# Performance work log

Measured on AMD Instinct MI355X. Metric: run time of the kernel, lower is better.

## Reference

```python
import jax, jax.numpy as jnp
import numpy as np

TOP_K_PERCENT = 0.7


def setup_inputs() -> dict:
    key = jax.random.key(0)
    k1, k2, k3, k4 = jax.random.split(key, 4)
    B, C, H, W = 4, 19, 512, 1024
    logits = jax.random.normal(k1, (B, C, H, W), dtype=jnp.float32)
    labels = jax.random.randint(k2, (B, H, W), 0, C, dtype=jnp.int64)
    smooth_labels = jax.random.uniform(k3, (B, C, H, W), dtype=jnp.float32)
    weight2 = jax.random.uniform(k4, (C,), dtype=jnp.float32)
    return {"logits": logits, "labels": labels, "smooth_labels": smooth_labels, "weight2": weight2}


def reference(logits, labels, smooth_labels, weight2):
    # Fused equivalent of the per-class loop:
    #   cum[b,h,w] = sum_c smooth[b,c,h,w] * weight2[c] * (-log_softmax(logits)[b,c,h,w])
    # (ignore_label=-1 never matches any class index, so no masking occurs.)
    logp = jax.nn.log_softmax(logits, axis=1)  # [B,C,H,W]
    w = weight2[None, :, None, None]
    pixel_losses_2 = -(smooth_labels * w * logp).sum(axis=1)  # [B,H,W]
    flat = pixel_losses_2.reshape(-1)
    k = int(TOP_K_PERCENT * flat.shape[0])  # static shape -> python int
    top_vals, _ = jax.lax.top_k(flat, k)
    return top_vals.mean()
```

## Files before the change

kernel.cpp:

```cpp
#include <hip/hip_runtime.h>

#define NPIX     2097152
#define NT4      524288
#define NCH      19
#define KSEL     1468006u
#define NBLK     2048
#define H1B      4096
#define H23B     1024
#define NHB      128

#define OFF_ROWS  (NPIX*4)
#define OFF_COMB1 (OFF_ROWS + NHB*H1B*4)
#define OFF_COMB2 (OFF_COMB1 + H1B*4)
#define OFF_PART  (OFF_COMB2 + H23B*4)
#define OFF_CTRL  (OFF_PART + NBLK*8)

struct Ctrl { unsigned p1, n1, p2, n2, T, r2; };

__global__ __launch_bounds__(256) void k_loss(
    const float* __restrict__ logits, const float* __restrict__ smooth,
    const float* __restrict__ wgt, float* __restrict__ loss)
{
    int tid = blockIdx.x * 256 + threadIdx.x;
    int img = tid >> 17;
    int rem = tid & 131071;
    const float4* L = (const float4*)logits + (size_t)img * (NCH * 131072) + rem;
    const float4* S = (const float4*)smooth + (size_t)img * (NCH * 131072) + rem;

    float4 xb[4], sb[4];
    #pragma unroll
    for (int i = 0; i < 4; ++i) {
        xb[i] = L[(size_t)i * 131072];
        sb[i] = S[(size_t)i * 131072];
    }

    float m0 = -3.4e38f, m1 = -3.4e38f, m2 = -3.4e38f, m3 = -3.4e38f;
    float s0 = 0.f, s1 = 0.f, s2 = 0.f, s3 = 0.f;
    float sw0 = 0.f, sw1 = 0.f, sw2 = 0.f, sw3 = 0.f;
    float swl0 = 0.f, swl1 = 0.f, swl2 = 0.f, swl3 = 0.f;

    #pragma unroll
    for (int c = 0; c < NCH; ++c) {
        float4 xv = xb[c & 3];
        float4 sv = sb[c & 3];
        if (c + 4 < NCH) {
            xb[c & 3] = L[(size_t)(c + 4) * 131072];
            sb[c & 3] = S[(size_t)(c + 4) * 131072];
        }
        float wc = wgt[c];

        float n0 = fmaxf(m0, xv.x), n1 = fmaxf(m1, xv.y);
        float n2 = fmaxf(m2, xv.z), n3 = fmaxf(m3, xv.w);
        s0 = s0 * __expf(m0 - n0) + __expf(xv.x - n0);
        s1 = s1 * __expf(m1 - n1) + __expf(xv.y - n1);
        s2 = s2 * __expf(m2 - n2) + __expf(xv.z - n2);
        s3 = s3 * __expf(m3 - n3) + __expf(xv.w - n3);
        m0 = n0; m1 = n1; m2 = n2; m3 = n3;

        float t0 = sv.x * wc, t1 = sv.y * wc, t2 = sv.z * wc, t3 = sv.w * wc;
        sw0 += t0; sw1 += t1; sw2 += t2; sw3 += t3;
        swl0 += t0 * xv.x; swl1 += t1 * xv.y;
        swl2 += t2 * xv.z; swl3 += t3 * xv.w;
    }

    float l0 = fmaxf((m0 + __logf(s0)) * sw0 - swl0, 0.f);
    float l1 = fmaxf((m1 + __logf(s1)) * sw1 - swl1, 0.f);
    float l2 = fmaxf((m2 + __logf(s2)) * sw2 - swl2, 0.f);
    float l3 = fmaxf((m3 + __logf(s3)) * sw3 - swl3, 0.f);

    ((float4*)loss)[tid] = make_float4(l0, l1, l2, l3);
}

__global__ __launch_bounds__(256) void k_hist1(
    const uint4* __restrict__ lossbits, unsigned* __restrict__ rows)
{
    __shared__ unsigned h[H1B];
    int t = threadIdx.x;
    #pragma unroll
    for (int j = t; j < H1B; j += 256) h[j] = 0;
    __syncthreads();
    int base = blockIdx.x * (NT4 / NHB);
    for (int i = t; i < NT4 / NHB; i += 256) {
        uint4 v = lossbits[base + i];
        atomicAdd(&h[v.x >> 20], 1u);
        atomicAdd(&h[v.y >> 20], 1u);
        atomicAdd(&h[v.z >> 20], 1u);
        atomicAdd(&h[v.w >> 20], 1u);
    }
    __syncthreads();
    for (int j = t; j < H1B; j += 256)
        rows[blockIdx.x * H1B + j] = h[j];
}

__global__ __launch_bounds__(256) void k_histr(
    const uint4* __restrict__ lossbits, const Ctrl* __restrict__ ctrl,
    unsigned* __restrict__ rows, int lvl)
{
    __shared__ unsigned h[H23B];
    unsigned pref = (lvl == 0) ? ctrl->p1 : ctrl->p2;
    int ms = (lvl == 0) ? 20 : 10;
    int bs = (lvl == 0) ? 10 : 0;
    int t = threadIdx.x;
    #pragma unroll
    for (int j = t; j < H23B; j += 256) h[j] = 0;
    __syncthreads();
    int base = blockIdx.x * (NT4 / NHB);
    for (int i = t; i < NT4 / NHB; i += 256) {
        uint4 v = lossbits[base + i];
        if ((v.x >> ms) == pref) atomicAdd(&h[(v.x >> bs) & 1023u], 1u);
        if ((v.y >> ms) == pref) atomicAdd(&h[(v.y >> bs) & 1023u], 1u);
        if ((v.z >> ms) == pref) atomicAdd(&h[(v.z >> bs) & 1023u], 1u);
        if ((v.w >> ms) == pref) atomicAdd(&h[(v.w >> bs) & 1023u], 1u);
    }
    __syncthreads();
    for (int j = t; j < H23B; j += 256)
        rows[blockIdx.x * H23B + j] = h[j];
}

__global__ __launch_bounds__(256) void k_reduce(
    const unsigned* __restrict__ rows, unsigned* __restrict__ comb, int nbins)
{
    int i = blockIdx.x * 256 + threadIdx.x;
    unsigned s = 0;
    for (int b = 0; b < NHB; ++b) s += rows[b * nbins + i];
    comb[i] = s;
}

__global__ __launch_bounds__(256) void k_sel1(
    const unsigned* __restrict__ comb, Ctrl* __restrict__ ctrl)
{
    __shared__ unsigned bins[H1B];
    __shared__ unsigned cs[256];
    __shared__ unsigned sh_t0, sh_base;
    int t = threadIdx.x;
    for (int j = t; j < H1B; j += 256) bins[j] = comb[j];
    __syncthreads();
    unsigned sum = 0;
    #pragma unroll
    for (int j = 0; j < 16; ++j) sum += bins[t * 16 + j];
    cs[t] = sum; __syncthreads();
    for (int off = 1; off < 256; off <<= 1) {
        unsigned v = (t + off < 256) ? cs[t + off] : 0u;
        __syncthreads();
        cs[t] += v;
        __syncthreads();
    }
    unsigned St = cs[t], Sn = (t < 255) ? cs[t + 1] : 0u;
    if (St >= KSEL && Sn < KSEL) { sh_t0 = (unsigned)t; sh_base = Sn; }
    __syncthreads();
    if (t == 0) {
        unsigned cum = sh_base;
        for (int b = (int)sh_t0 * 16 + 15;; --b) {
            unsigned c = bins[b];
            if (cum + c >= KSEL) { ctrl->p1 = (unsigned)b; ctrl->n1 = KSEL - cum; break; }
            cum += c;
        }
    }
}

__global__ __launch_bounds__(256) void k_selr(
    const unsigned* __restrict__ comb, Ctrl* __restrict__ ctrl, int lvl)
{
    __shared__ unsigned bins[H23B];
    __shared__ unsigned cs[256];
    __shared__ unsigned sh_t0, sh_base;
    int t = threadIdx.x;
    unsigned need = (lvl == 0) ? ctrl->n1 : ctrl->n2;
    unsigned pref = (lvl == 0) ? ctrl->p1 : ctrl->p2;
    for (int j = t; j < H23B; j += 256) bins[j] = comb[j];
    __syncthreads();
    unsigned sum = bins[t*4] + bins[t*4+1] + bins[t*4+2] + bins[t*4+3];
    cs[t] = sum; __syncthreads();
    for (int off = 1; off < 256; off <<= 1) {
        unsigned v = (t + off < 256) ? cs[t + off] : 0u;
        __syncthreads();
        cs[t] += v;
        __syncthreads();
    }
    unsigned St = cs[t], Sn = (t < 255) ? cs[t + 1] : 0u;
    if (St >= need && Sn < need) { sh_t0 = (unsigned)t; sh_base = Sn; }
    __syncthreads();
    if (t == 0) {
        unsigned cum = sh_base;
        for (int b = (int)sh_t0 * 4 + 3;; --b) {
            unsigned c = bins[b];
            if (cum + c >= need) {
                if (lvl == 0) { ctrl->p2 = (pref << 10) | (unsigned)b; ctrl->n2 = need - cum; }
                else          { ctrl->T  = (pref << 10) | (unsigned)b; ctrl->r2 = need - cum; }
                break;
            }
            cum += c;
        }
    }
}

__global__ __launch_bounds__(256) void k_sum(
    const uint4* __restrict__ lossbits, const Ctrl* __restrict__ ctrl,
    double* __restrict__ partials)
{
    unsigned T = ctrl->T;
    int tid = blockIdx.x * 256 + threadIdx.x;
    uint4 v = lossbits[tid];
    double acc = 0.0;
    if (v.x > T) acc += (double)__uint_as_float(v.x);
    if (v.y > T) acc += (double)__uint_as_float(v.y);
    if (v.z > T) acc += (double)__uint_as_float(v.z);
    if (v.w > T) acc += (double)__uint_as_float(v.w);
    #pragma unroll
    for (int off = 32; off > 0; off >>= 1) acc += __shfl_down(acc, off, 64);
    __shared__ double wsum[4];
    int lane = threadIdx.x & 63, wid = threadIdx.x >> 6;
    if (lane == 0) wsum[wid] = acc;
    __syncthreads();
    if (threadIdx.x == 0)
        partials[blockIdx.x] = wsum[0] + wsum[1] + wsum[2] + wsum[3];
}

__global__ __launch_bounds__(256) void k_final(
    const double* __restrict__ partials, const Ctrl* __restrict__ ctrl,
    float* __restrict__ out)
{
    double acc = 0.0;
    for (int i = threadIdx.x; i < NBLK; i += 256) acc += partials[i];
    #pragma unroll
    for (int off = 32; off > 0; off >>= 1) acc += __shfl_down(acc, off, 64);
    __shared__ double wsum[4];
    int lane = threadIdx.x & 63, wid = threadIdx.x >> 6;
    if (lane == 0) wsum[wid] = acc;
    __syncthreads();
    if (threadIdx.x == 0) {
        double tot = wsum[0] + wsum[1] + wsum[2] + wsum[3];
        tot += (double)ctrl->r2 * (double)__uint_as_float(ctrl->T);
        out[0] = (float)(tot / (double)KSEL);
    }
}

extern "C" void kernel_launch(void* const* d_in, const int* in_sizes, int n_in,
                              void* d_out, int out_size, void* d_ws, size_t ws_size,
                              hipStream_t stream)
{
    const float* logits = (const float*)d_in[0];
    const float* smooth = (const float*)d_in[2];
    const float* wgt    = (const float*)d_in[3];

    char* ws = (char*)d_ws;
    float*    loss     = (float*)ws;
    unsigned* rows     = (unsigned*)(ws + OFF_ROWS);
    unsigned* comb1    = (unsigned*)(ws + OFF_COMB1);
    unsigned* comb2    = (unsigned*)(ws + OFF_COMB2);
    double*   partials = (double*)(ws + OFF_PART);
    Ctrl*     ctrl     = (Ctrl*)(ws + OFF_CTRL);
    const uint4* lb    = (const uint4*)loss;

    k_loss  <<<NBLK, 256, 0, stream>>>(logits, smooth, wgt, loss);
    k_hist1 <<<NHB, 256, 0, stream>>>(lb, rows);
    k_reduce<<<H1B / 256, 256, 0, stream>>>(rows, comb1, H1B);
    k_sel1  <<<1, 256, 0, stream>>>(comb1, ctrl);
    k_histr <<<NHB, 256, 0, stream>>>(lb, ctrl, rows, 0);
    k_reduce<<<H23B / 256, 256, 0, stream>>>(rows, comb2, H23B);
    k_selr  <<<1, 256, 0, stream>>>(comb2, ctrl, 0);
    k_histr <<<NHB, 256, 0, stream>>>(lb, ctrl, rows, 1);
    k_reduce<<<H23B / 256, 256, 0, stream>>>(rows, comb2, H23B);
    k_selr  <<<1, 256, 0, stream>>>(comb2, ctrl, 1);
    k_sum   <<<NBLK, 256, 0, stream>>>(lb, ctrl, partials);
    k_final <<<1, 256, 0, stream>>>(partials, ctrl, (float*)d_out);
}
```

Baseline: 377.9 us.

## Fuse radix-select passes, use global atomics for histograms, merge final sum

Restructures the top-k radix select pipeline. Per-block histogram rows and the separate reduce kernels are replaced by global atomic accumulation, with the bins zeroed inside the loss kernel. The third histogram pass is fused with the above-threshold sum, and the final selection is folded into the finish kernel, cutting the launch count from twelve to seven and dropping one full read of the loss array. The loss kernel now handles two pixels per thread (float2) across more blocks, and histogram grids grow to 512 blocks. The tradeoff is contention on the global atomics.

```diff
diff --git a/kernel.cpp b/kernel.cpp
--- a/kernel.cpp
+++ b/kernel.cpp
@@ -1,87 +1,86 @@
 #include <hip/hip_runtime.h>
 
-#define NPIX     2097152
-#define NT4      524288
-#define NCH      19
-#define KSEL     1468006u
-#define NBLK     2048
-#define H1B      4096
-#define H23B     1024
-#define NHB      128
-
-#define OFF_ROWS  (NPIX*4)
-#define OFF_COMB1 (OFF_ROWS + NHB*H1B*4)
+#define NPIX 2097152
+#define NT2  1048576
+#define NT4  524288
+#define NCH  19
+#define CPL2 262144
+#define KSEL 1468006u
+#define LBLK 4096
+#define HB   512
+#define H1B  4096
+#define H2B  1024
+
+#define OFF_COMB1 (NPIX*4)
 #define OFF_COMB2 (OFF_COMB1 + H1B*4)
-#define OFF_PART  (OFF_COMB2 + H23B*4)
-#define OFF_CTRL  (OFF_PART + NBLK*8)
-
-struct Ctrl { unsigned p1, n1, p2, n2, T, r2; };
-
-__global__ __launch_bounds__(256) void k_loss(
+#define OFF_PART  (OFF_COMB2 + H2B*4)
+#define OFF_CTRL  (OFF_PART + HB*8)
+
+struct Ctrl { unsigned p1, n1, p2, n2; };
+
+__global__ __launch_bounds__(256, 8) void k_loss(
     const float* __restrict__ logits, const float* __restrict__ smooth,
-    const float* __restrict__ wgt, float* __restrict__ loss)
-{
+    const float* __restrict__ wgt, float* __restrict__ loss,
+    unsigned* __restrict__ combz)
+{
+    if (blockIdx.x == 0) {
+        for (int j = threadIdx.x; j < H1B + H2B; j += 256) combz[j] = 0u;
+    }
     int tid = blockIdx.x * 256 + threadIdx.x;
-    int img = tid >> 17;
-    int rem = tid & 131071;
-    const float4* L = (const float4*)logits + (size_t)img * (NCH * 131072) + rem;
-    const float4* S = (const float4*)smooth + (size_t)img * (NCH * 131072) + rem;
-
-    float4 xb[4], sb[4];
+    int img = tid >> 18;
+    int rem = tid & (CPL2 - 1);
+    const float2* L = (const float2*)logits + (size_t)img * (NCH * CPL2) + rem;
+    const float2* S = (const float2*)smooth + (size_t)img * (NCH * CPL2) + rem;
+
+    float2 xb[4], sb[4];
     #pragma unroll
     for (int i = 0; i < 4; ++i) {
-        xb[i] = L[(size_t)i * 131072];
-        sb[i] = S[(size_t)i * 131072];
-    }
-
-    float m0 = -3.4e38f, m1 = -3.4e38f, m2 = -3.4e38f, m3 = -3.4e38f;
-    float s0 = 0.f, s1 = 0.f, s2 = 0.f, s3 = 0.f;
-    float sw0 = 0.f, sw1 = 0.f, sw2 = 0.f, sw3 = 0.f;
-    float swl0 = 0.f, swl1 = 0.f, swl2 = 0.f, swl3 = 0.f;
+        xb[i] = L[(size_t)i * CPL2];
+        sb[i] = S[(size_t)i * CPL2];
+    }
+
+    float m0 = -3.4e38f, m1 = -3.4e38f;
+    float s0 = 0.f, s1 = 0.f;
+    float sw0 = 0.f, sw1 = 0.f;
+    float swl0 = 0.f, swl1 = 0.f;
 
     #pragma unroll
     for (int c = 0; c < NCH; ++c) {
-        float4 xv = xb[c & 3];
-        float4 sv = sb[c & 3];
+        float2 xv = xb[c & 3];
+        float2 sv = sb[c & 3];
         if (c + 4 < NCH) {
-            xb[c & 3] = L[(size_t)(c + 4) * 131072];
-            sb[c & 3] = S[(size_t)(c + 4) * 131072];
+            xb[c & 3] = L[(size_t)(c + 4) * CPL2];
+            sb[c & 3] = S[(size_t)(c + 4) * CPL2];
         }
         float wc = wgt[c];
 
         float n0 = fmaxf(m0, xv.x), n1 = fmaxf(m1, xv.y);
-        float n2 = fmaxf(m2, xv.z), n3 = fmaxf(m3, xv.w);
         s0 = s0 * __expf(m0 - n0) + __expf(xv.x - n0);
         s1 = s1 * __expf(m1 - n1) + __expf(xv.y - n1);
-        s2 = s2 * __expf(m2 - n2) + __expf(xv.z - n2);
-        s3 = s3 * __expf(m3 - n3) + __expf(xv.w - n3);
-        m0 = n0; m1 = n1; m2 = n2; m3 = n3;
-
-        float t0 = sv.x * wc, t1 = sv.y * wc, t2 = sv.z * wc, t3 = sv.w * wc;
-        sw0 += t0; sw1 += t1; sw2 += t2; sw3 += t3;
+        m0 = n0; m1 = n1;
+
+        float t0 = sv.x * wc, t1 = sv.y * wc;
+        sw0 += t0; sw1 += t1;
         swl0 += t0 * xv.x; swl1 += t1 * xv.y;
-        swl2 += t2 * xv.z; swl3 += t3 * xv.w;
     }
 
     float l0 = fmaxf((m0 + __logf(s0)) * sw0 - swl0, 0.f);
     float l1 = fmaxf((m1 + __logf(s1)) * sw1 - swl1, 0.f);
-    float l2 = fmaxf((m2 + __logf(s2)) * sw2 - swl2, 0.f);
-    float l3 = fmaxf((m3 + __logf(s3)) * sw3 - swl3, 0.f);
-
-    ((float4*)loss)[tid] = make_float4(l0, l1, l2, l3);
+    ((float2*)loss)[tid] = make_float2(l0, l1);
 }
 
 __global__ __launch_bounds__(256) void k_hist1(
-    const uint4* __restrict__ lossbits, unsigned* __restrict__ rows)
+    const uint4* __restrict__ lb, unsigned* __restrict__ comb1)
 {
     __shared__ unsigned h[H1B];
     int t = threadIdx.x;
     #pragma unroll
     for (int j = t; j < H1B; j += 256) h[j] = 0;
     __syncthreads();
-    int base = blockIdx.x * (NT4 / NHB);
-    for (int i = t; i < NT4 / NHB; i += 256) {
-        uint4 v = lossbits[base + i];
+    int base = blockIdx.x * (NT4 / HB);
+    #pragma unroll
+    for (int i = 0; i < NT4 / HB / 256; ++i) {
+        uint4 v = lb[base + i * 256 + t];
         atomicAdd(&h[v.x >> 20], 1u);
         atomicAdd(&h[v.y >> 20], 1u);
         atomicAdd(&h[v.z >> 20], 1u);
@@ -89,41 +88,7 @@
     }
     __syncthreads();
     for (int j = t; j < H1B; j += 256)
-        rows[blockIdx.x * H1B + j] = h[j];
-}
-
-__global__ __launch_bounds__(256) void k_histr(
-    const uint4* __restrict__ lossbits, const Ctrl* __restrict__ ctrl,
-    unsigned* __restrict__ rows, int lvl)
-{
-    __shared__ unsigned h[H23B];
-    unsigned pref = (lvl == 0) ? ctrl->p1 : ctrl->p2;
-    int ms = (lvl == 0) ? 20 : 10;
-    int bs = (lvl == 0) ? 10 : 0;
-    int t = threadIdx.x;
-    #pragma unroll
-    for (int j = t; j < H23B; j += 256) h[j] = 0;
-    __syncthreads();
-    int base = blockIdx.x * (NT4 / NHB);
-    for (int i = t; i < NT4 / NHB; i += 256) {
-        uint4 v = lossbits[base + i];
-        if ((v.x >> ms) == pref) atomicAdd(&h[(v.x >> bs) & 1023u], 1u);
-        if ((v.y >> ms) == pref) atomicAdd(&h[(v.y >> bs) & 1023u], 1u);
-        if ((v.z >> ms) == pref) atomicAdd(&h[(v.z >> bs) & 1023u], 1u);
-        if ((v.w >> ms) == pref) atomicAdd(&h[(v.w >> bs) & 1023u], 1u);
-    }
-    __syncthreads();
-    for (int j = t; j < H23B; j += 256)
-        rows[blockIdx.x * H23B + j] = h[j];
-}
-
-__global__ __launch_bounds__(256) void k_reduce(
-    const unsigned* __restrict__ rows, unsigned* __restrict__ comb, int nbins)
-{
-    int i = blockIdx.x * 256 + threadIdx.x;
-    unsigned s = 0;
-    for (int b = 0; b < NHB; ++b) s += rows[b * nbins + i];
-    comb[i] = s;
+        if (h[j]) atomicAdd(&comb1[j], h[j]);
 }
 
 __global__ __launch_bounds__(256) void k_sel1(
@@ -158,16 +123,39 @@
     }
 }
 
-__global__ __launch_bounds__(256) void k_selr(
-    const unsigned* __restrict__ comb, Ctrl* __restrict__ ctrl, int lvl)
-{
-    __shared__ unsigned bins[H23B];
+__global__ __launch_bounds__(256) void k_hist2(
+    const uint4* __restrict__ lb, const Ctrl* __restrict__ ctrl,
+    unsigned* __restrict__ comb2)
+{
+    __shared__ unsigned h[H2B];
+    unsigned p1 = ctrl->p1;
+    int t = threadIdx.x;
+    #pragma unroll
+    for (int j = t; j < H2B; j += 256) h[j] = 0;
+    __syncthreads();
+    int base = blockIdx.x * (NT4 / HB);
+    #pragma unroll
+    for (int i = 0; i < NT4 / HB / 256; ++i) {
+        uint4 v = lb[base + i * 256 + t];
+        if ((v.x >> 20) == p1) atomicAdd(&h[(v.x >> 10) & 1023u], 1u);
+        if ((v.y >> 20) == p1) atomicAdd(&h[(v.y >> 10) & 1023u], 1u);
+        if ((v.z >> 20) == p1) atomicAdd(&h[(v.z >> 10) & 1023u], 1u);
+        if ((v.w >> 20) == p1) atomicAdd(&h[(v.w >> 10) & 1023u], 1u);
+    }
+    __syncthreads();
+    for (int j = t; j < H2B; j += 256)
+        if (h[j]) atomicAdd(&comb2[j], h[j]);
+}
+
+__global__ __launch_bounds__(256) void k_sel2(
+    unsigned* __restrict__ comb2, Ctrl* __restrict__ ctrl)
+{
+    __shared__ unsigned bins[H2B];
     __shared__ unsigned cs[256];
     __shared__ unsigned sh_t0, sh_base;
     int t = threadIdx.x;
-    unsigned need = (lvl == 0) ? ctrl->n1 : ctrl->n2;
-    unsigned pref = (lvl == 0) ? ctrl->p1 : ctrl->p2;
-    for (int j = t; j < H23B; j += 256) bins[j] = comb[j];
+    unsigned need = ctrl->n1, pref = ctrl->p1;
+    for (int j = t; j < H2B; j += 256) { bins[j] = comb2[j]; comb2[j] = 0u; }
     __syncthreads();
     unsigned sum = bins[t*4] + bins[t*4+1] + bins[t*4+2] + bins[t*4+3];
     cs[t] = sum; __syncthreads();
@@ -185,8 +173,8 @@
         for (int b = (int)sh_t0 * 4 + 3;; --b) {
             unsigned c = bins[b];
             if (cum + c >= need) {
-                if (lvl == 0) { ctrl->p2 = (pref << 10) | (unsigned)b; ctrl->n2 = need - cum; }
-                else          { ctrl->T  = (pref << 10) | (unsigned)b; ctrl->r2 = need - cum; }
+                ctrl->p2 = (pref << 10) | (unsigned)b;
+                ctrl->n2 = need - cum;
                 break;
             }
             cum += c;
@@ -194,43 +182,92 @@
     }
 }
 
-__global__ __launch_bounds__(256) void k_sum(
-    const uint4* __restrict__ lossbits, const Ctrl* __restrict__ ctrl,
-    double* __restrict__ partials)
-{
-    unsigned T = ctrl->T;
-    int tid = blockIdx.x * 256 + threadIdx.x;
-    uint4 v = lossbits[tid];
+__global__ __launch_bounds__(256) void k_hist3(
+    const uint4* __restrict__ lb, const Ctrl* __restrict__ ctrl,
+    unsigned* __restrict__ comb2, double* __restrict__ partials)
+{
+    __shared__ unsigned h[H2B];
+    __shared__ double wsum[4];
+    unsigned p2 = ctrl->p2;
+    int t = threadIdx.x;
+    #pragma unroll
+    for (int j = t; j < H2B; j += 256) h[j] = 0;
+    __syncthreads();
+    int base = blockIdx.x * (NT4 / HB);
     double acc = 0.0;
-    if (v.x > T) acc += (double)__uint_as_float(v.x);
-    if (v.y > T) acc += (double)__uint_as_float(v.y);
-    if (v.z > T) acc += (double)__uint_as_float(v.z);
-    if (v.w > T) acc += (double)__uint_as_float(v.w);
+    #pragma unroll
+    for (int i = 0; i < NT4 / HB / 256; ++i) {
+        uint4 v = lb[base + i * 256 + t];
+        unsigned px = v.x >> 10, py = v.y >> 10, pz = v.z >> 10, pw = v.w >> 10;
+        if (px == p2) atomicAdd(&h[v.x & 1023u], 1u);
+        else if (px > p2) acc += (double)__uint_as_float(v.x);
+        if (py == p2) atomicAdd(&h[v.y & 1023u], 1u);
+        else if (py > p2) acc += (double)__uint_as_float(v.y);
+        if (pz == p2) atomicAdd(&h[v.z & 1023u], 1u);
+        else if (pz > p2) acc += (double)__uint_as_float(v.z);
+        if (pw == p2) atomicAdd(&h[v.w & 1023u], 1u);
+        else if (pw > p2) acc += (double)__uint_as_float(v.w);
+    }
+    __syncthreads();
+    for (int j = t; j < H2B; j += 256)
+        if (h[j]) atomicAdd(&comb2[j], h[j]);
     #pragma unroll
     for (int off = 32; off > 0; off >>= 1) acc += __shfl_down(acc, off, 64);
+    int lane = t & 63, wid = t >> 6;
+    if (lane == 0) wsum[wid] = acc;
+    __syncthreads();
+    if (t == 0) partials[blockIdx.x] = wsum[0] + wsum[1] + wsum[2] + wsum[3];
+}
+
+__global__ __launch_bounds__(256) void k_fin(
+    const unsigned* __restrict__ comb2, const double* __restrict__ partials,
+    const Ctrl* __restrict__ ctrl, float* __restrict__ out)
+{
+    __shared__ unsigned bins[H2B];
+    __shared__ unsigned cs[256];
+    __shared__ unsigned sh_t0, sh_base, sh_b3, sh_r2;
     __shared__ double wsum[4];
-    int lane = threadIdx.x & 63, wid = threadIdx.x >> 6;
+    int t = threadIdx.x;
+    unsigned need = ctrl->n2, p2 = ctrl->p2;
+    for (int j = t; j < H2B; j += 256) bins[j] = comb2[j];
+    __syncthreads();
+    unsigned sum = bins[t*4] + bins[t*4+1] + bins[t*4+2] + bins[t*4+3];
+    cs[t] = sum; __syncthreads();
+    for (int off = 1; off < 256; off <<= 1) {
+        unsigned v = (t + off < 256) ? cs[t + off] : 0u;
+        __syncthreads();
+        cs[t] += v;
+        __syncthreads();
+    }
+    unsigned St = cs[t], Sn = (t < 255) ? cs[t + 1] : 0u;
+    if (St >= need && Sn < need) { sh_t0 = (unsigned)t; sh_base = Sn; }
+    __syncthreads();
+    if (t == 0) {
+        unsigned cum = sh_base;
+        for (int b = (int)sh_t0 * 4 + 3;; --b) {
+            unsigned c = bins[b];
+            if (cum + c >= need) { sh_b3 = (unsigned)b; sh_r2 = need - cum; break; }
+            cum += c;
+        }
+    }
+    __syncthreads();
+    int b3 = (int)sh_b3;
+    double acc = partials[t] + partials[t + 256];
+    #pragma unroll
+    for (int k = 0; k < 4; ++k) {
+        int b = t * 4 + k;
+        if (b > b3 && bins[b])
+            acc += (double)bins[b] * (double)__uint_as_float((p2 << 10) | (unsigned)b);
+    }
+    #pragma unroll
+    for (int off = 32; off > 0; off >>= 1) acc += __shfl_down(acc, off, 64);
+    int lane = t & 63, wid = t >> 6;
     if (lane == 0) wsum[wid] = acc;
     __syncthreads();
-    if (threadIdx.x == 0)
-        partials[blockIdx.x] = wsum[0] + wsum[1] + wsum[2] + wsum[3];
-}
-
-__global__ __launch_bounds__(256) void k_final(
-    const double* __restrict__ partials, const Ctrl* __restrict__ ctrl,
-    float* __restrict__ out)
-{
-    double acc = 0.0;
-    for (int i = threadIdx.x; i < NBLK; i += 256) acc += partials[i];
-    #pragma unroll
-    for (int off = 32; off > 0; off >>= 1) acc += __shfl_down(acc, off, 64);
-    __shared__ double wsum[4];
-    int lane = threadIdx.x & 63, wid = threadIdx.x >> 6;
-    if (lane == 0) wsum[wid] = acc;
-    __syncthreads();
-    if (threadIdx.x == 0) {
+    if (t == 0) {
         double tot = wsum[0] + wsum[1] + wsum[2] + wsum[3];
-        tot += (double)ctrl->r2 * (double)__uint_as_float(ctrl->T);
+        unsigned Tb = (p2 << 10) | sh_b3;
+        tot += (double)sh_r2 * (double)__uint_as_float(Tb);
         out[0] = (float)(tot / (double)KSEL);
     }
 }
@@ -245,23 +282,17 @@
 
     char* ws = (char*)d_ws;
     float*    loss     = (float*)ws;
-    unsigned* rows     = (unsigned*)(ws + OFF_ROWS);
     unsigned* comb1    = (unsigned*)(ws + OFF_COMB1);
     unsigned* comb2    = (unsigned*)(ws + OFF_COMB2);
     double*   partials = (double*)(ws + OFF_PART);
     Ctrl*     ctrl     = (Ctrl*)(ws + OFF_CTRL);
     const uint4* lb    = (const uint4*)loss;
 
-    k_loss  <<<NBLK, 256, 0, stream>>>(logits, smooth, wgt, loss);
-    k_hist1 <<<NHB, 256, 0, stream>>>(lb, rows);
-    k_reduce<<<H1B / 256, 256, 0, stream>>>(rows, comb1, H1B);
-    k_sel1  <<<1, 256, 0, stream>>>(comb1, ctrl);
-    k_histr <<<NHB, 256, 0, stream>>>(lb, ctrl, rows, 0);
-    k_reduce<<<H23B / 256, 256, 0, stream>>>(rows, comb2, H23B);
-    k_selr  <<<1, 256, 0, stream>>>(comb2, ctrl, 0);
-    k_histr <<<NHB, 256, 0, stream>>>(lb, ctrl, rows, 1);
-    k_reduce<<<H23B / 256, 256, 0, stream>>>(rows, comb2, H23B);
-    k_selr  <<<1, 256, 0, stream>>>(comb2, ctrl, 1);
-    k_sum   <<<NBLK, 256, 0, stream>>>(lb, ctrl, partials);
-    k_final <<<1, 256, 0, stream>>>(partials, ctrl, (float*)d_out);
-}
+    k_loss <<<LBLK, 256, 0, stream>>>(logits, smooth, wgt, loss, comb1);
+    k_hist1<<<HB,   256, 0, stream>>>(lb, comb1);
+    k_sel1 <<<1,    256, 0, stream>>>(comb1, ctrl);
+    k_hist2<<<HB,   256, 0, stream>>>(lb, ctrl, comb2);
+    k_sel2 <<<1,    256, 0, stream>>>(comb2, ctrl);
+    k_hist3<<<HB,   256, 0, stream>>>(lb, ctrl, comb2, partials);
+    k_fin  <<<1,    256, 0, stream>>>(comb2, partials, ctrl, (float*)d_out);
+}
```

Result: slower. 392.6 us (+3.9%).
